# Kernel optimization log

Measured on AMD Instinct MI355X. Metric: run time of the kernel, lower is better.

## Reference

```python
import jax, jax.numpy as jnp
import numpy as np

N_NODES = 50000
N_EDGES = 800000
D_FEAT = 128
D_EMB = 128


def setup_inputs() -> dict:
    key = jax.random.key(0)
    k1, k2, k3, k4, k5 = jax.random.split(key, 5)
    feature = jax.random.normal(k1, (N_NODES, D_FEAT), dtype=jnp.float32)
    edge_src = jax.random.randint(k2, (N_EDGES,), 0, N_NODES, dtype=jnp.int32)
    edge_dst = jax.random.randint(k3, (N_EDGES,), 0, N_NODES, dtype=jnp.int32)
    edge_w = jax.random.uniform(k4, (N_EDGES,), dtype=jnp.float32)
    # reset_parameters: uniform(-stdv, stdv), stdv = 1/sqrt(embedding_size)
    stdv = 1.0 / np.sqrt(D_EMB)
    weight = jax.random.uniform(k5, (D_FEAT, D_EMB), dtype=jnp.float32,
                                minval=-stdv, maxval=stdv)
    return {"feature": feature, "edge_src": edge_src, "edge_dst": edge_dst,
            "edge_w": edge_w, "weight": weight}


def reference(feature, edge_src, edge_dst, edge_w, weight):
    # spmm(adj, feature): out[dst] += w * feature[src]
    msgs = edge_w[:, None] * feature[edge_src]          # [E, D_FEAT]
    agg = jax.ops.segment_sum(msgs, edge_dst, num_segments=feature.shape[0])
    # residual blend then dense projection
    blended = 0.5 * agg + 0.5 * feature                  # [N, D_FEAT]
    return blended @ weight                              # [N, D_EMB]
```

## Files before the change

kernel.cpp:

```cpp
#include <hip/hip_runtime.h>

#define N_NODES 50000
#define N_EDGES 800000
#define D 128
#define NBUCK 196
#define CAP 4800
#define CHUNK 4096
#define PA_BLKS ((N_EDGES + CHUNK - 1) / CHUNK)
#define FB_BLKS 12500
#define WT_BLKS 64
#define SLOTS 16

typedef __attribute__((ext_vector_type(8))) short short8;
typedef __attribute__((ext_vector_type(4))) float f32x4;

__device__ __forceinline__ unsigned short f2bf(float f) {
    unsigned u = __float_as_uint(f);
    u += 0x7fff + ((u >> 16) & 1);
    return (unsigned short)(u >> 16);
}

__global__ __launch_bounds__(256) void prep_passA(
    const float2* __restrict__ feat2, unsigned* __restrict__ fb,
    const float* __restrict__ W, unsigned short* __restrict__ Wt,
    const int* __restrict__ esrc, const int* __restrict__ edst,
    const float* __restrict__ ew, int* __restrict__ gcur,
    uint2* __restrict__ tmp) {
    __shared__ int lh[NBUCK], lbase[NBUCK], lcur[NBUCK];
    int blk = blockIdx.x, t = threadIdx.x;

    if (blk >= PA_BLKS) {
        int b2 = blk - PA_BLKS;
        if (b2 < FB_BLKS) {
            int i = b2 * 256 + t;
            float2 f = feat2[i];
            fb[i] = (unsigned)f2bf(f.x) | ((unsigned)f2bf(f.y) << 16);
        } else {
            int idx = (b2 - FB_BLKS) * 256 + t;
            int n = idx >> 7, k = idx & 127;
            Wt[idx] = f2bf(W[k * 128 + n]);
        }
        return;
    }

    for (int i = t; i < NBUCK; i += 256) lh[i] = 0;
    __syncthreads();
    int e0 = blk * CHUNK;
    unsigned key[16];
    float wv[16];
#pragma unroll
    for (int j = 0; j < 16; ++j) {
        int e = e0 + j * 256 + t;
        if (e < N_EDGES) {
            int src = esrc[e], dd = edst[e];
            key[j] = (unsigned)src | ((unsigned)(dd & 255) << 16) |
                     ((unsigned)(dd >> 8) << 24);
            wv[j] = ew[e];
            atomicAdd(&lh[dd >> 8], 1);
        } else key[j] = 0xff000000u;
    }
    __syncthreads();
    for (int i = t; i < NBUCK; i += 256) {
        lbase[i] = atomicAdd(&gcur[i], lh[i]);
        lcur[i] = 0;
    }
    __syncthreads();
#pragma unroll
    for (int j = 0; j < 16; ++j) {
        int b = key[j] >> 24;
        if (b < NBUCK) {
            int r = atomicAdd(&lcur[b], 1);
            tmp[(size_t)b * CAP + lbase[b] + r] =
                make_uint2(key[j] & 0x00ffffffu, __float_as_uint(wv[j]));
        }
    }
}

__global__ __launch_bounds__(256) void passB(const int* __restrict__ gcur,
                                             const uint2* __restrict__ tmp,
                                             int* __restrict__ offsets,
                                             uint2* __restrict__ sw) {
    __shared__ int gb[NBUCK];
    __shared__ int hist[256], ps[256];
    __shared__ int sbase;
    int b = blockIdx.x, t = threadIdx.x;
    for (int i = t; i < NBUCK; i += 256) gb[i] = gcur[i];
    hist[t] = 0;
    __syncthreads();
    if (t == 0) {
        int run = 0;
        for (int i = 0; i < b; ++i) run += gb[i];
        sbase = run;
    }
    __syncthreads();
    int base = sbase, cnt = gb[b];
    const uint2* seg = tmp + (size_t)b * CAP;

    for (int i = t; i < cnt; i += 256) atomicAdd(&hist[seg[i].x >> 16], 1);
    __syncthreads();
    int h = hist[t];
    ps[t] = h;
    __syncthreads();
    for (int off = 1; off < 256; off <<= 1) {
        int x = (t >= off) ? ps[t - off] : 0;
        __syncthreads();
        ps[t] += x;
        __syncthreads();
    }
    int o = base + ps[t] - h;
    int node = b * 256 + t;
    if (node < N_NODES) offsets[node] = o;
    if (b == NBUCK - 1 && t == 0) offsets[N_NODES] = N_EDGES;
    __syncthreads();
    hist[t] = o;
    __syncthreads();
    for (int i = t; i < cnt; i += 256) {
        uint2 u = seg[i];
        int pos = atomicAdd(&hist[u.x >> 16], 1);
        sw[pos] = make_uint2(u.x & 0xffffu, u.y);
    }
}

__global__ __launch_bounds__(256) void agg_gemm(const int* __restrict__ offsets,
                                                const uint2* __restrict__ sw,
                                                const unsigned* __restrict__ fb,
                                                const unsigned short* __restrict__ Wt,
                                                float* __restrict__ out) {
    __shared__ unsigned Arows[16][68];
    __shared__ unsigned gbuf[4][SLOTS][64];
    int wave = threadIdx.x >> 6;
    int lane = threadIdx.x & 63;
    int row0 = blockIdx.x * 16;
    unsigned* gb = &gbuf[wave][0][0];

#pragma unroll 1
    for (int i = 0; i < 4; ++i) {
        int n = __builtin_amdgcn_readfirstlane(row0 + wave * 4 + i);
        int b = offsets[n], e2 = offsets[n + 1];
        unsigned us = fb[(size_t)n * 64 + lane];
        float ax = 0.f, ay = 0.f;
        int e = b;
        while (e < e2) {
            int cnt = e2 - e;
            cnt = cnt > SLOTS ? SLOTS : cnt;
#pragma unroll 1
            for (int j = 0; j < cnt; ++j) {
                unsigned src = sw[e + j].x;
                const unsigned* g = fb + (size_t)src * 64 + lane;
                __builtin_amdgcn_global_load_lds(g, gb + j * 64, 4, 0, 0);
            }
            __builtin_amdgcn_s_waitcnt(0x0f70);
#pragma unroll 1
            for (int j = 0; j < cnt; ++j) {
                float w = __uint_as_float(sw[e + j].y);
                unsigned u = gb[j * 64 + lane];
                ax += w * __uint_as_float(u << 16);
                ay += w * __uint_as_float(u & 0xffff0000u);
            }
            e += cnt;
        }
        float rx = 0.5f * (ax + __uint_as_float(us << 16));
        float ry = 0.5f * (ay + __uint_as_float(us & 0xffff0000u));
        Arows[wave * 4 + i][lane] = (unsigned)f2bf(rx) | ((unsigned)f2bf(ry) << 16);
    }
    __syncthreads();

    int quad = lane >> 4;
    int col  = lane & 15;
    short8 a[4];
#pragma unroll
    for (int kk = 0; kk < 4; ++kk)
        a[kk] = *reinterpret_cast<const short8*>(&Arows[col][kk * 16 + quad * 4]);

#pragma unroll
    for (int ii = 0; ii < 2; ++ii) {
        int n0 = wave * 2 + ii;
        const short8* bp = reinterpret_cast<const short8*>(Wt) + ((n0 * 16 + col) * 16 + quad);
        f32x4 acc = {0.f, 0.f, 0.f, 0.f};
        acc = __builtin_amdgcn_mfma_f32_16x16x32_bf16(a[0], bp[0],  acc, 0, 0, 0);
        acc = __builtin_amdgcn_mfma_f32_16x16x32_bf16(a[1], bp[4],  acc, 0, 0, 0);
        acc = __builtin_amdgcn_mfma_f32_16x16x32_bf16(a[2], bp[8],  acc, 0, 0, 0);
        acc = __builtin_amdgcn_mfma_f32_16x16x32_bf16(a[3], bp[12], acc, 0, 0, 0);
#pragma unroll
        for (int rr = 0; rr < 4; ++rr)
            out[(size_t)(row0 + quad * 4 + rr) * D + n0 * 16 + col] = acc[rr];
    }
}

extern "C" void kernel_launch(void* const* d_in, const int* in_sizes, int n_in,
                              void* d_out, int out_size, void* d_ws, size_t ws_size,
                              hipStream_t stream) {
    const float* feat = (const float*)d_in[0];
    const int*   esrc = (const int*)d_in[1];
    const int*   edst = (const int*)d_in[2];
    const float* ew   = (const float*)d_in[3];
    const float* W    = (const float*)d_in[4];
    float*       out  = (float*)d_out;

    char* ws = (char*)d_ws;
    uint2*          sw      = (uint2*)(ws + 0);
    unsigned*       fb      = (unsigned*)(ws + 6400000);
    int*            offsets = (int*)(ws + 19200000);
    unsigned short* Wt      = (unsigned short*)(ws + 19400064);
    int*            gcur    = (int*)(ws + 19432832);
    uint2* tmp = (uint2*)d_out;

    hipMemsetAsync(gcur, 0, NBUCK * sizeof(int), stream);
    prep_passA<<<PA_BLKS + FB_BLKS + WT_BLKS, 256, 0, stream>>>(
        (const float2*)feat, fb, W, Wt, esrc, edst, ew, gcur, tmp);
    passB<<<NBUCK, 256, 0, stream>>>(gcur, tmp, offsets, sw);
    agg_gemm<<<N_NODES / 16, 256, 0, stream>>>(offsets, sw, fb, Wt, out);
}
```

Baseline: 154.4 us.

## Gather two edges per wave with 8-byte loads and parallel bucket prefix scan

The aggregation loop no longer stages neighbor rows through LDS with global_load_lds and a full waitcnt. Instead each wave loads 16 edge records at once and broadcasts them with readlane. Each half-wave then gathers a different source row with 8-byte loads, so two edges are processed per iteration, and the halves are combined with a cross-lane shuffle. In passB, the serial per-block prefix over bucket counts becomes a parallel shared-memory scan. This trades LDS staging and sync stalls for direct register gathers, with more independent loads in flight per unrolled iteration.

```diff
diff --git a/kernel.cpp b/kernel.cpp
--- a/kernel.cpp
+++ b/kernel.cpp
@@ -9,7 +9,6 @@
 #define PA_BLKS ((N_EDGES + CHUNK - 1) / CHUNK)
 #define FB_BLKS 12500
 #define WT_BLKS 64
-#define SLOTS 16
 
 typedef __attribute__((ext_vector_type(8))) short short8;
 typedef __attribute__((ext_vector_type(4))) float f32x4;
@@ -19,6 +18,8 @@
     u += 0x7fff + ((u >> 16) & 1);
     return (unsigned short)(u >> 16);
 }
+__device__ __forceinline__ float lo16f(unsigned u) { return __uint_as_float(u << 16); }
+__device__ __forceinline__ float hi16f(unsigned u) { return __uint_as_float(u & 0xffff0000u); }
 
 __global__ __launch_bounds__(256) void prep_passA(
     const float2* __restrict__ feat2, unsigned* __restrict__ fb,
@@ -80,20 +81,23 @@
                                              const uint2* __restrict__ tmp,
                                              int* __restrict__ offsets,
                                              uint2* __restrict__ sw) {
-    __shared__ int gb[NBUCK];
     __shared__ int hist[256], ps[256];
-    __shared__ int sbase;
+    __shared__ int sbase, scnt;
     int b = blockIdx.x, t = threadIdx.x;
-    for (int i = t; i < NBUCK; i += 256) gb[i] = gcur[i];
+
+    int gv = (t < NBUCK) ? gcur[t] : 0;
+    ps[t] = gv;
+    __syncthreads();
+    for (int off = 1; off < 256; off <<= 1) {
+        int x = (t >= off) ? ps[t - off] : 0;
+        __syncthreads();
+        ps[t] += x;
+        __syncthreads();
+    }
+    if (t == b) { sbase = ps[t] - gv; scnt = gv; }
     hist[t] = 0;
     __syncthreads();
-    if (t == 0) {
-        int run = 0;
-        for (int i = 0; i < b; ++i) run += gb[i];
-        sbase = run;
-    }
-    __syncthreads();
-    int base = sbase, cnt = gb[b];
+    int base = sbase, cnt = scnt;
     const uint2* seg = tmp + (size_t)b * CAP;
 
     for (int i = t; i < cnt; i += 256) atomicAdd(&hist[seg[i].x >> 16], 1);
@@ -127,41 +131,69 @@
                                                 const unsigned short* __restrict__ Wt,
                                                 float* __restrict__ out) {
     __shared__ unsigned Arows[16][68];
-    __shared__ unsigned gbuf[4][SLOTS][64];
     int wave = threadIdx.x >> 6;
     int lane = threadIdx.x & 63;
+    int m = lane & 31;
+    bool low = lane < 32;
     int row0 = blockIdx.x * 16;
-    unsigned* gb = &gbuf[wave][0][0];
+    const uint2* fb2 = (const uint2*)fb;
 
 #pragma unroll 1
     for (int i = 0; i < 4; ++i) {
         int n = __builtin_amdgcn_readfirstlane(row0 + wave * 4 + i);
         int b = offsets[n], e2 = offsets[n + 1];
-        unsigned us = fb[(size_t)n * 64 + lane];
-        float ax = 0.f, ay = 0.f;
+        uint2 sf = fb2[(size_t)n * 32 + m];
+        float4 acc = make_float4(0.f, 0.f, 0.f, 0.f);
         int e = b;
-        while (e < e2) {
+        for (; e + 16 <= e2; e += 16) {
+            uint2 sv = sw[e + (lane & 15)];
+#pragma unroll
+            for (int j = 0; j < 8; ++j) {
+                unsigned sA = __builtin_amdgcn_readlane(sv.x, 2 * j);
+                unsigned sB = __builtin_amdgcn_readlane(sv.x, 2 * j + 1);
+                unsigned wA = __builtin_amdgcn_readlane(sv.y, 2 * j);
+                unsigned wB = __builtin_amdgcn_readlane(sv.y, 2 * j + 1);
+                unsigned src = low ? sA : sB;
+                float w = __uint_as_float(low ? wA : wB);
+                uint2 dv = fb2[(size_t)src * 32 + m];
+                acc.x += w * lo16f(dv.x);
+                acc.y += w * hi16f(dv.x);
+                acc.z += w * lo16f(dv.y);
+                acc.w += w * hi16f(dv.y);
+            }
+        }
+        if (e < e2) {
             int cnt = e2 - e;
-            cnt = cnt > SLOTS ? SLOTS : cnt;
+            uint2 sv = sw[e + ((lane & 15) < cnt ? (lane & 15) : cnt - 1)];
 #pragma unroll 1
-            for (int j = 0; j < cnt; ++j) {
-                unsigned src = sw[e + j].x;
-                const unsigned* g = fb + (size_t)src * 64 + lane;
-                __builtin_amdgcn_global_load_lds(g, gb + j * 64, 4, 0, 0);
+            for (int j = 0; 2 * j < cnt; ++j) {
+                unsigned sA = __builtin_amdgcn_readlane(sv.x, 2 * j);
+                unsigned wA = __builtin_amdgcn_readlane(sv.y, 2 * j);
+                bool hasB = (2 * j + 1) < cnt;
+                unsigned sB = hasB ? __builtin_amdgcn_readlane(sv.x, 2 * j + 1) : sA;
+                unsigned wB = hasB ? __builtin_amdgcn_readlane(sv.y, 2 * j + 1) : 0u;
+                unsigned src = low ? sA : sB;
+                float w = __uint_as_float(low ? wA : wB);
+                uint2 dv = fb2[(size_t)src * 32 + m];
+                acc.x += w * lo16f(dv.x);
+                acc.y += w * hi16f(dv.x);
+                acc.z += w * lo16f(dv.y);
+                acc.w += w * hi16f(dv.y);
             }
-            __builtin_amdgcn_s_waitcnt(0x0f70);
-#pragma unroll 1
-            for (int j = 0; j < cnt; ++j) {
-                float w = __uint_as_float(sw[e + j].y);
-                unsigned u = gb[j * 64 + lane];
-                ax += w * __uint_as_float(u << 16);
-                ay += w * __uint_as_float(u & 0xffff0000u);
-            }
-            e += cnt;
-        }
-        float rx = 0.5f * (ax + __uint_as_float(us << 16));
-        float ry = 0.5f * (ay + __uint_as_float(us & 0xffff0000u));
-        Arows[wave * 4 + i][lane] = (unsigned)f2bf(rx) | ((unsigned)f2bf(ry) << 16);
+        }
+        acc.x += __shfl_xor(acc.x, 32);
+        acc.y += __shfl_xor(acc.y, 32);
+        acc.z += __shfl_xor(acc.z, 32);
+        acc.w += __shfl_xor(acc.w, 32);
+        if (low) {
+            float r0 = 0.5f * (acc.x + lo16f(sf.x));
+            float r1 = 0.5f * (acc.y + hi16f(sf.x));
+            float r2 = 0.5f * (acc.z + lo16f(sf.y));
+            float r3 = 0.5f * (acc.w + hi16f(sf.y));
+            int r = wave * 4 + i;
+            Arows[r][2 * m]     = (unsigned)f2bf(r0) | ((unsigned)f2bf(r1) << 16);
+            Arows[r][2 * m + 1] = (unsigned)f2bf(r2) | ((unsigned)f2bf(r3) << 16);
+        }
     }
     __syncthreads();
 
```

Result: no change. 154.8 us (+0.2%).
